# Kernel tuning notes

Hardware: AMD Instinct MI355X
Metric: run time of the kernel (lower is better)

The kernel has to match this reference:

```python
import jax, jax.numpy as jnp
import numpy as np

EMBED_DIM = 1024
NUM_HEADS = 16
HEAD_DIM = EMBED_DIM // NUM_HEADS


def setup_inputs() -> dict:
    key = jax.random.key(0)
    ks = jax.random.split(key, 11)
    B, S, D = 2, 2048, EMBED_DIM
    s = 1.0 / np.sqrt(D)
    inp = {
        "q": jax.random.normal(ks[0], (B, S, D), jnp.float32),
        "k": jax.random.normal(ks[1], (B, S, D), jnp.float32),
        "v": jax.random.normal(ks[2], (B, S, D), jnp.float32),
        # Linear params stored as (in, out) so y = x @ W + b
        "wq": jax.random.uniform(ks[3], (D, D), jnp.float32, -s, s),
        "bq": jax.random.uniform(ks[4], (D,), jnp.float32, -s, s),
        "wk": jax.random.uniform(ks[5], (D, D), jnp.float32, -s, s),
        "bk": jax.random.uniform(ks[6], (D,), jnp.float32, -s, s),
        "wv": jax.random.uniform(ks[7], (D, D), jnp.float32, -s, s),
        "bv": jax.random.uniform(ks[8], (D,), jnp.float32, -s, s),
        "wo": jax.random.uniform(ks[9], (D, D), jnp.float32, -s, s),
        "bo": jax.random.uniform(ks[10], (D,), jnp.float32, -s, s),
    }
    return inp


def reference(q, k, v, wq, bq, wk, bk, wv, bv, wo, bo):
    B, S, D = q.shape
    H, Hd = NUM_HEADS, HEAD_DIM
    temperature = Hd ** 0.5

    def proj(x, w, b):
        # (B, S, D) -> (B, H, S, Hd)
        y = x @ w + b
        return y.reshape(B, S, H, Hd).transpose(0, 2, 1, 3)

    qh = proj(q, wq, bq)
    kh = proj(k, wk, bk)
    vh = proj(v, wv, bv)

    # naive attention with materialized [B, H, S, S] scores (faithful to source)
    scores = jnp.einsum("bhqd,bhkd->bhqk", qh / temperature, kh)
    attn = jax.nn.softmax(scores, axis=-1)
    ctx = jnp.einsum("bhqk,bhkd->bhqd", attn, vh)

    ctx = ctx.transpose(0, 2, 1, 3).reshape(B, S, D)
    out = ctx @ wo + bo
    return out, attn
```

## Files before the change

kernel.cpp:

```cpp
#include <hip/hip_runtime.h>

#define S_   2048
#define D_   1024

typedef __attribute__((ext_vector_type(8))) __bf16 bf16x8;
typedef __attribute__((ext_vector_type(4))) __bf16 bf16x4;
typedef __attribute__((ext_vector_type(4))) float f32x4;
typedef __attribute__((ext_vector_type(4))) float float4v;
typedef __attribute__((ext_vector_type(2))) unsigned int u32x2;
typedef __attribute__((ext_vector_type(4))) unsigned int u32x4;

#define XQ_OFF   0
#define XK_OFF   4194304
#define XV_OFF   8388608
#define WQT_OFF  12582912
#define WKT_OFF  13631488
#define WVT_OFF  14680064
#define WOT_OFF  15728640
#define QH_OFF   16777216
#define KH_OFF   20971520
#define VHT_OFF  25165824
#define CTX_OFF  29360128
#define WS_BYTES 67108864ULL

#if __has_builtin(__builtin_amdgcn_exp2f)
#define EXP2(x) __builtin_amdgcn_exp2f(x)
#else
#define EXP2(x) __expf((x) * 0.69314718056f)
#endif
#define QSCALE 0.1803368801f

__device__ __forceinline__ unsigned short f2b(float f) {
  unsigned u = __builtin_bit_cast(unsigned, f);
  u += 0x7fffu + ((u >> 16) & 1u);
  return (unsigned short)(u >> 16);
}
__device__ __forceinline__ float b2f(unsigned s) {
  return __builtin_bit_cast(float, s << 16);
}

__global__ __launch_bounds__(256) void cvt_all(const float* __restrict__ q,
    const float* __restrict__ k, const float* __restrict__ v,
    const float* __restrict__ wq, const float* __restrict__ wk,
    const float* __restrict__ wv, const float* __restrict__ wo,
    short* __restrict__ ws) {
  __shared__ float tile[32][33];
  int b = blockIdx.x, tid = threadIdx.x;
  if (b < 12288) {
    int y = b >> 12, x = b & 4095;
    const float* src = (y == 0) ? q : (y == 1) ? k : v;
    short* dst = ws + (size_t)y * 4194304;
    size_t t = (size_t)x * 256 + tid;
    float4v f = *(const float4v*)(src + t * 4);
    u32x2 p;
    p[0] = (unsigned)f2b(f[0]) | ((unsigned)f2b(f[1]) << 16);
    p[1] = (unsigned)f2b(f[2]) | ((unsigned)f2b(f[3]) << 16);
    *(u32x2*)(dst + t * 4) = p;
    return;
  }
  int b2 = b - 12288;
  int z = b2 >> 10, rem = b2 & 1023;
  int by = rem >> 5, bx = rem & 31;
  const float* W = (z == 0) ? wq : (z == 1) ? wk : (z == 2) ? wv : wo;
  short* Wt = ws + WQT_OFF + (size_t)z * 1048576;
  int tx = tid & 31, ty = tid >> 5;
#pragma unroll
  for (int i = 0; i < 4; ++i)
    tile[ty + i * 8][tx] =
        W[(size_t)(by * 32 + ty + i * 8) * D_ + bx * 32 + tx];
  __syncthreads();
#pragma unroll
  for (int i = 0; i < 4; ++i)
    Wt[(size_t)(bx * 32 + ty + i * 8) * D_ + by * 32 + tx] =
        (short)f2b(tile[tx][ty + i * 8]);
}

__device__ __forceinline__ void stage_tile(const short* __restrict__ g,
                                           short* l, int w, int lane) {
  int lrow = lane >> 3, lcol = (lane & 7) * 8;
#pragma unroll
  for (int c = 0; c < 4; ++c) {
    int seg = c * 4 + w;
    const short* gp = g + (size_t)(seg * 8 + lrow) * 1024 + lcol;
    short* lp = l + seg * 512 + lane * 8;
    __builtin_amdgcn_global_load_lds(
        (const __attribute__((address_space(1))) void*)gp,
        (__attribute__((address_space(3))) void*)lp, 16, 0, 0);
  }
}

__global__ __launch_bounds__(256) void gemm_bf16(short* __restrict__ ws,
    const float* __restrict__ bq, const float* __restrict__ bk,
    const float* __restrict__ bv, const float* __restrict__ bo,
    float* __restrict__ out, int mode_base) {
  const int tid = threadIdx.x, lane = tid & 63, w = tid >> 6;
  const int wm = w >> 1, wn = w & 1;
  const int ln15 = lane & 15, g = lane >> 4;
  const int bm = blockIdx.y, bn = blockIdx.x;
  const int mode = (mode_base == 3) ? 3 : (int)blockIdx.z;

  const short* A; const short* Bt; const float* bias;
  if (mode == 0)      { A = ws + XQ_OFF;  Bt = ws + WQT_OFF; bias = bq; }
  else if (mode == 1) { A = ws + XK_OFF;  Bt = ws + WKT_OFF; bias = bk; }
  else if (mode == 2) { A = ws + XV_OFF;  Bt = ws + WVT_OFF; bias = bv; }
  else                { A = ws + CTX_OFF; Bt = ws + WOT_OFF; bias = bo; }

  __shared__ short smem[2][2][8192];
  short (*sA)[8192] = smem[0];
  short (*sB)[8192] = smem[1];

  f32x4 acc[4][4] = {};

  const short* Ab = A + (size_t)bm * 128 * 1024;
  const short* Bb = Bt + (size_t)bn * 128 * 1024;

  stage_tile(Ab, sA[0], w, lane);
  stage_tile(Bb, sB[0], w, lane);
  __syncthreads();

  int cur = 0;
#pragma unroll 1
  for (int kt = 0; kt < 16; ++kt) {
    if (kt < 15) {
      stage_tile(Ab + (kt + 1) * 64, sA[cur ^ 1], w, lane);
      stage_tile(Bb + (kt + 1) * 64, sB[cur ^ 1], w, lane);
    }
#pragma unroll
    for (int kk = 0; kk < 2; ++kk) {
      bf16x8 af[4], bfr[4];
#pragma unroll
      for (int m = 0; m < 4; ++m)
        af[m] = *(const bf16x8*)&sA[cur][(wm * 64 + m * 16 + ln15) * 64 + kk * 32 + g * 8];
#pragma unroll
      for (int n = 0; n < 4; ++n)
        bfr[n] = *(const bf16x8*)&sB[cur][(wn * 64 + n * 16 + ln15) * 64 + kk * 32 + g * 8];
#pragma unroll
      for (int m = 0; m < 4; ++m)
#pragma unroll
        for (int n = 0; n < 4; ++n)
          acc[m][n] = __builtin_amdgcn_mfma_f32_16x16x32_bf16(af[m], bfr[n], acc[m][n], 0, 0, 0);
    }
    __syncthreads();
    cur ^= 1;
  }

  float bb[4];
#pragma unroll
  for (int n = 0; n < 4; ++n) bb[n] = bias[bn * 128 + wn * 64 + n * 16 + ln15];

  if (mode == 3) {
#pragma unroll
    for (int m = 0; m < 4; ++m) {
      int row0 = bm * 128 + wm * 64 + m * 16 + g * 4;
#pragma unroll
      for (int n = 0; n < 4; ++n) {
        int col = bn * 128 + wn * 64 + n * 16 + ln15;
#pragma unroll
        for (int r = 0; r < 4; ++r)
          out[(size_t)(row0 + r) * 1024 + col] = acc[m][n][r] + bb[n];
      }
    }
    return;
  }

  float sc = (mode == 0) ? QSCALE : 1.0f;
  short (*tile)[136] = (short(*)[136])smem;
#pragma unroll
  for (int m = 0; m < 4; ++m)
#pragma unroll
    for (int n = 0; n < 4; ++n)
#pragma unroll
      for (int r = 0; r < 4; ++r)
        tile[wm * 64 + m * 16 + g * 4 + r][wn * 64 + n * 16 + ln15] =
            (short)f2b((acc[m][n][r] + bb[n]) * sc);
  __syncthreads();

  if (mode == 2) {
    int dcol = tid >> 1, sh = (tid & 1) * 64;
    int colg = bn * 128 + dcol, h = colg >> 6, hd = colg & 63;
    int b = bm >> 4, sblk = bm & 15;
    short* dst = ws + VHT_OFF +
                 ((size_t)((b * 16 + h) * 16 + sblk)) * 8192 + hd * 128 + sh;
#pragma unroll
    for (int j = 0; j < 8; ++j) {
      u32x4 pk;
#pragma unroll
      for (int q = 0; q < 4; ++q) {
        unsigned lo = (unsigned short)tile[sh + j * 8 + q * 2][dcol];
        unsigned hi = (unsigned short)tile[sh + j * 8 + q * 2 + 1][dcol];
        pk[q] = lo | (hi << 16);
      }
      *(u32x4*)(dst + j * 8) = pk;
    }
  } else {
    int r = tid >> 1, sh = (tid & 1) * 64;
    int colg = bn * 128 + sh, h = colg >> 6;
    int sg = bm * 128 + r, b = sg >> 11, sl = sg & 2047;
    short* dst = ws + ((mode == 0) ? QH_OFF : KH_OFF) +
                 (((size_t)(b * 16 + h)) * 2048 + sl) * 64;
#pragma unroll
    for (int j = 0; j < 8; ++j)
      *(u32x4*)(dst + j * 8) = *(const u32x4*)&tile[r][sh + j * 8];
  }
}

__global__ __launch_bounds__(512) void attn_k(short* __restrict__ ws,
                                              float* __restrict__ attn) {
  const int tid = threadIdx.x, lane = tid & 63, w = tid >> 6;
  const int ln15 = lane & 15, g = lane >> 4, ln7 = lane & 7;
  int bid = blockIdx.x;
  int qt = (bid >> 3) & 15;
  int bh = (bid & 7) + 8 * (bid >> 7);
  const int q0 = qt * 128;

  const short* Q  = ws + QH_OFF  + ((size_t)bh * 2048 + q0) * 64;
  const short* K  = ws + KH_OFF  + (size_t)bh * 2048 * 64;
  const short* Vt = ws + VHT_OFF + (size_t)bh * 131072;

  __shared__ short sStage[6][4096];
  __shared__ short Pbig[128][264];

  const int srow = tid >> 3, sc = tid & 7;
  const int scsw = sc ^ (srow & 7);
  const int sdst = tid * 8;

#define STAGE_K2(kt)                                                          \
  __builtin_amdgcn_global_load_lds(                                           \
      (const __attribute__((address_space(1))) void*)(K + ((kt) * 64 + srow) * 64 + scsw * 8),         \
      (__attribute__((address_space(3))) void*)(&sStage[(kt) % 3][sdst]), 16, 0, 0)
#define STAGE_V2(kt)                                                          \
  __builtin_amdgcn_global_load_lds(                                           \
      (const __attribute__((address_space(1))) void*)(Vt + ((kt) >> 1) * 8192 + srow * 128 + ((kt) & 1) * 64 + scsw * 8), \
      (__attribute__((address_space(3))) void*)(&sStage[3 + (kt) % 3][sdst]), 16, 0, 0)
#define STAGE1(t1, b)                                                         \
  do {                                                                        \
    __builtin_amdgcn_global_load_lds(                                         \
        (const __attribute__((address_space(1))) void*)(K + ((t1) * 128 + srow) * 64 + scsw * 8),      \
        (__attribute__((address_space(3))) void*)(&sStage[(b)][sdst]), 16, 0, 0);                      \
    __builtin_amdgcn_global_load_lds(                                         \
        (const __attribute__((address_space(1))) void*)(K + ((t1) * 128 + 64 + srow) * 64 + scsw * 8), \
        (__attribute__((address_space(3))) void*)(&sStage[3 + (b)][sdst]), 16, 0, 0);                  \
  } while (0)

  bf16x8 qf0 = *(const bf16x8*)&Q[(w * 16 + ln15) * 64 + g * 8];
  bf16x8 qf1 = *(const bf16x8*)&Q[(w * 16 + ln15) * 64 + 32 + g * 8];

  STAGE1(0, 0);
  asm volatile("s_waitcnt vmcnt(0)" ::: "memory");
  __builtin_amdgcn_s_barrier();

  float ps0 = 0.f, ps1 = 0.f;
#pragma unroll 1
  for (int t = 0; t < 16; ++t) {
    int b = t & 1;
    if (t < 15) STAGE1(t + 1, b ^ 1);
#pragma unroll
    for (int m = 0; m < 8; ++m) {
      const short* kbase =
          &sStage[(m >> 2) * 3 + b][((m * 16 + ln15) & 63) * 64];
      bf16x8 ka0 = *(const bf16x8*)&kbase[(g ^ ln7) * 8];
      bf16x8 ka1 = *(const bf16x8*)&kbase[((4 + g) ^ ln7) * 8];
      f32x4 c = {0.f, 0.f, 0.f, 0.f};
      c = __builtin_amdgcn_mfma_f32_16x16x32_bf16(ka0, qf0, c, 0, 0, 0);
      c = __builtin_amdgcn_mfma_f32_16x16x32_bf16(ka1, qf1, c, 0, 0, 0);
      ps0 += EXP2(c[0]) + EXP2(c[1]);
      ps1 += EXP2(c[2]) + EXP2(c[3]);
    }
    asm volatile("s_waitcnt vmcnt(0)" ::: "memory");
    __builtin_amdgcn_s_barrier();
  }
  float ps = ps0 + ps1;
  ps += __shfl_xor(ps, 16, 64);
  ps += __shfl_xor(ps, 32, 64);
  float ri = 1.0f / ps;

  f32x4 cacc[4] = {};

  STAGE_K2(0);
  STAGE_V2(0);
  STAGE_K2(1);
  STAGE_V2(1);
  asm volatile("s_waitcnt vmcnt(2)" ::: "memory");
  __builtin_amdgcn_s_barrier();

#pragma unroll 1
  for (int s = 0; s < 8; ++s) {
#pragma unroll
    for (int j = 0; j < 4; ++j) {
      const int kt = s * 4 + j;
      const int ktm3 = kt % 3;
      if (kt < 30) {
        STAGE_K2(kt + 2);
        STAGE_V2(kt + 2);
      }
#pragma unroll
      for (int m = 0; m < 4; ++m) {
        const short* kbase = &sStage[ktm3][(m * 16 + ln15) * 64];
        bf16x8 ka0 = *(const bf16x8*)&kbase[(g ^ ln7) * 8];
        bf16x8 ka1 = *(const bf16x8*)&kbase[((4 + g) ^ ln7) * 8];
        f32x4 c = {0.f, 0.f, 0.f, 0.f};
        c = __builtin_amdgcn_mfma_f32_16x16x32_bf16(ka0, qf0, c, 0, 0, 0);
        c = __builtin_amdgcn_mfma_f32_16x16x32_bf16(ka1, qf1, c, 0, 0, 0);
        bf16x4 pb;
        pb[0] = (__bf16)(EXP2(c[0]) * ri);
        pb[1] = (__bf16)(EXP2(c[1]) * ri);
        pb[2] = (__bf16)(EXP2(c[2]) * ri);
        pb[3] = (__bf16)(EXP2(c[3]) * ri);
        *(bf16x4*)&Pbig[w * 16 + ln15][j * 64 + m * 16 + g * 4] = pb;
      }
      asm volatile("s_waitcnt lgkmcnt(0)" ::: "memory");
      __builtin_amdgcn_sched_barrier(0);

#pragma unroll
      for (int kk = 0; kk < 2; ++kk) {
        bf16x8 pa =
            *(const bf16x8*)&Pbig[w * 16 + ln15][j * 64 + kk * 32 + g * 8];
#pragma unroll
        for (int n = 0; n < 4; ++n) {
          const short* vbase = &sStage[3 + ktm3][(n * 16 + ln15) * 64];
          bf16x8 vb = *(const bf16x8*)&vbase[((kk * 4 + g) ^ ln7) * 8];
          cacc[n] =
              __builtin_amdgcn_mfma_f32_16x16x32_bf16(pa, vb, cacc[n], 0, 0, 0);
        }
      }

      if (kt >= 30) {
        asm volatile("s_waitcnt vmcnt(0)" ::: "memory");
      } else if (j == 0 && s > 0) {
        asm volatile("s_waitcnt vmcnt(18)" ::: "memory");
      } else {
        asm volatile("s_waitcnt vmcnt(2)" ::: "memory");
      }
      __builtin_amdgcn_s_barrier();
    }

    float* ab = attn + ((size_t)(bh * 2048 + q0 + w * 16)) * 2048 + s * 256 +
                lane * 4;
#pragma unroll
    for (int r = 0; r < 16; ++r) {
      u32x2 pv = *(const u32x2*)&Pbig[w * 16 + r][lane * 4];
      float4v o;
      o[0] = b2f(pv[0] & 0xffffu);
      o[1] = b2f(pv[0] >> 16);
      o[2] = b2f(pv[1] & 0xffffu);
      o[3] = b2f(pv[1] >> 16);
      *(float4v*)(ab + (size_t)r * 2048) = o;
    }
  }

  {
    short* Pw = &Pbig[w * 16][0];
#pragma unroll
    for (int n = 0; n < 4; ++n)
#pragma unroll
      for (int r = 0; r < 4; ++r)
        Pw[(g * 4 + r) * 264 + n * 16 + ln15] = (short)f2b(cacc[n][r]);
    asm volatile("s_waitcnt lgkmcnt(0)" ::: "memory");
    __builtin_amdgcn_sched_barrier(0);
    int b = bh >> 4, h = bh & 15;
    int row = lane >> 3, col = (lane & 7) * 8;
#pragma unroll
    for (int i = 0; i < 2; ++i) {
      int q = q0 + w * 16 + i * 8 + row;
      u32x4 pk = *(const u32x4*)&Pw[(i * 8 + row) * 264 + col];
      *(u32x4*)&ws[CTX_OFF + ((size_t)(b * 2048 + q)) * 1024 + h * 64 + col] = pk;
    }
  }
#undef STAGE_K2
#undef STAGE_V2
#undef STAGE1
}

extern "C" void kernel_launch(void* const* d_in, const int* in_sizes, int n_in,
                              void* d_out, int out_size, void* d_ws, size_t ws_size,
                              hipStream_t stream) {
  const float* q  = (const float*)d_in[0];
  const float* k  = (const float*)d_in[1];
  const float* v  = (const float*)d_in[2];
  const float* wq = (const float*)d_in[3];
  const float* bq = (const float*)d_in[4];
  const float* wk = (const float*)d_in[5];
  const float* bk = (const float*)d_in[6];
  const float* wv = (const float*)d_in[7];
  const float* bv = (const float*)d_in[8];
  const float* wo = (const float*)d_in[9];
  const float* bo = (const float*)d_in[10];
  float* out  = (float*)d_out;
  float* attn = out + 4194304;
  short* ws = (short*)d_ws;
  if (ws_size < WS_BYTES) return;

  cvt_all<<<dim3(16384), 256, 0, stream>>>(q, k, v, wq, wk, wv, wo, ws);
  gemm_bf16<<<dim3(8, 32, 3), 256, 0, stream>>>(ws, bq, bk, bv, bo, out, 0);
  attn_k<<<dim3(512), 512, 0, stream>>>(ws, attn);
  gemm_bf16<<<dim3(8, 32, 1), 256, 0, stream>>>(ws, bq, bk, bv, bo, out, 3);
}
```

Baseline: 294.9 us.

## Store Q/K/V in MFMA fragment order and load fragments directly from global

New measurement: 302.8 us. 2.7% more time.

```diff
diff --git a/kernel.cpp b/kernel.cpp
--- a/kernel.cpp
+++ b/kernel.cpp
@@ -175,99 +175,84 @@
             (short)f2b((acc[m][n][r] + bb[n]) * sc);
   __syncthreads();
 
-  if (mode == 2) {
-    int dcol = tid >> 1, sh = (tid & 1) * 64;
-    int colg = bn * 128 + dcol, h = colg >> 6, hd = colg & 63;
-    int b = bm >> 4, sblk = bm & 15;
-    short* dst = ws + VHT_OFF +
-                 ((size_t)((b * 16 + h) * 16 + sblk)) * 8192 + hd * 128 + sh;
-#pragma unroll
-    for (int j = 0; j < 8; ++j) {
+  const int bq_ = bm >> 4;
+  const int sml = bm & 15;
+  if (mode == 0) {
+    int h_out = tid >> 7, rt = (tid >> 4) & 7, h = (tid >> 3) & 1, sub = tid & 7;
+    int bh = bq_ * 16 + bn * 2 + h_out;
+    size_t base = QH_OFF + (((size_t)bh * 128 + sml * 8 + rt) * 2 + h) * 512;
+#pragma unroll
+    for (int i = 0; i < 8; ++i) {
+      int l = sub * 8 + i;
+      u32x4 v = *(const u32x4*)&tile[rt * 16 + (l & 15)]
+                                    [h_out * 64 + h * 32 + (l >> 4) * 8];
+      *(u32x4*)&ws[base + l * 8] = v;
+    }
+  } else if (mode == 1) {
+    int kt_l = tid >> 7, h_out = (tid >> 6) & 1, f = (tid >> 3) & 7, sub = tid & 7;
+    int bh = bq_ * 16 + bn * 2 + h_out;
+    size_t base = KH_OFF + (((size_t)bh * 32 + sml * 2 + kt_l) * 8 + f) * 512;
+#pragma unroll
+    for (int i = 0; i < 8; ++i) {
+      int l = sub * 8 + i;
+      u32x4 v = *(const u32x4*)&tile[kt_l * 64 + (f >> 1) * 16 + (l & 15)]
+                                    [h_out * 64 + (f & 1) * 32 + (l >> 4) * 8];
+      *(u32x4*)&ws[base + l * 8] = v;
+    }
+  } else {
+    int kt_l = tid >> 7, h_out = (tid >> 6) & 1, fv = (tid >> 3) & 7, sub = tid & 7;
+    int bh = bq_ * 16 + bn * 2 + h_out;
+    size_t base = VHT_OFF + (((size_t)bh * 32 + sml * 2 + kt_l) * 8 + fv) * 512;
+#pragma unroll
+    for (int i = 0; i < 8; ++i) {
+      int l = sub * 8 + i;
+      int hd = h_out * 64 + (fv >> 1) * 16 + (l & 15);
+      int s0 = kt_l * 64 + (fv & 1) * 32 + (l >> 4) * 8;
       u32x4 pk;
 #pragma unroll
-      for (int q = 0; q < 4; ++q) {
-        unsigned lo = (unsigned short)tile[sh + j * 8 + q * 2][dcol];
-        unsigned hi = (unsigned short)tile[sh + j * 8 + q * 2 + 1][dcol];
-        pk[q] = lo | (hi << 16);
+      for (int e2 = 0; e2 < 4; ++e2) {
+        unsigned lo = (unsigned short)tile[s0 + e2 * 2][hd];
+        unsigned hi = (unsigned short)tile[s0 + e2 * 2 + 1][hd];
+        pk[e2] = lo | (hi << 16);
       }
-      *(u32x4*)(dst + j * 8) = pk;
-    }
-  } else {
-    int r = tid >> 1, sh = (tid & 1) * 64;
-    int colg = bn * 128 + sh, h = colg >> 6;
-    int sg = bm * 128 + r, b = sg >> 11, sl = sg & 2047;
-    short* dst = ws + ((mode == 0) ? QH_OFF : KH_OFF) +
-                 (((size_t)(b * 16 + h)) * 2048 + sl) * 64;
-#pragma unroll
-    for (int j = 0; j < 8; ++j)
-      *(u32x4*)(dst + j * 8) = *(const u32x4*)&tile[r][sh + j * 8];
+      *(u32x4*)&ws[base + l * 8] = pk;
+    }
   }
 }
 
 __global__ __launch_bounds__(512) void attn_k(short* __restrict__ ws,
                                               float* __restrict__ attn) {
   const int tid = threadIdx.x, lane = tid & 63, w = tid >> 6;
-  const int ln15 = lane & 15, g = lane >> 4, ln7 = lane & 7;
+  const int ln15 = lane & 15, g = lane >> 4;
   int bid = blockIdx.x;
   int qt = (bid >> 3) & 15;
   int bh = (bid & 7) + 8 * (bid >> 7);
   const int q0 = qt * 128;
 
-  const short* Q  = ws + QH_OFF  + ((size_t)bh * 2048 + q0) * 64;
-  const short* K  = ws + KH_OFF  + (size_t)bh * 2048 * 64;
-  const short* Vt = ws + VHT_OFF + (size_t)bh * 131072;
-
-  __shared__ short sStage[6][4096];
+  const short* qhF = ws + QH_OFF + (((size_t)bh * 128 + qt * 8 + w) * 2) * 512;
+  const short* khF = ws + KH_OFF + (size_t)bh * 131072;
+  const short* vhF = ws + VHT_OFF + (size_t)bh * 131072;
+
   __shared__ short Pbig[128][264];
 
-  const int srow = tid >> 3, sc = tid & 7;
-  const int scsw = sc ^ (srow & 7);
-  const int sdst = tid * 8;
-
-#define STAGE_K2(kt)                                                          \
-  __builtin_amdgcn_global_load_lds(                                           \
-      (const __attribute__((address_space(1))) void*)(K + ((kt) * 64 + srow) * 64 + scsw * 8),         \
-      (__attribute__((address_space(3))) void*)(&sStage[(kt) % 3][sdst]), 16, 0, 0)
-#define STAGE_V2(kt)                                                          \
-  __builtin_amdgcn_global_load_lds(                                           \
-      (const __attribute__((address_space(1))) void*)(Vt + ((kt) >> 1) * 8192 + srow * 128 + ((kt) & 1) * 64 + scsw * 8), \
-      (__attribute__((address_space(3))) void*)(&sStage[3 + (kt) % 3][sdst]), 16, 0, 0)
-#define STAGE1(t1, b)                                                         \
-  do {                                                                        \
-    __builtin_amdgcn_global_load_lds(                                         \
-        (const __attribute__((address_space(1))) void*)(K + ((t1) * 128 + srow) * 64 + scsw * 8),      \
-        (__attribute__((address_space(3))) void*)(&sStage[(b)][sdst]), 16, 0, 0);                      \
-    __builtin_amdgcn_global_load_lds(                                         \
-        (const __attribute__((address_space(1))) void*)(K + ((t1) * 128 + 64 + srow) * 64 + scsw * 8), \
-        (__attribute__((address_space(3))) void*)(&sStage[3 + (b)][sdst]), 16, 0, 0);                  \
-  } while (0)
-
-  bf16x8 qf0 = *(const bf16x8*)&Q[(w * 16 + ln15) * 64 + g * 8];
-  bf16x8 qf1 = *(const bf16x8*)&Q[(w * 16 + ln15) * 64 + 32 + g * 8];
-
-  STAGE1(0, 0);
-  asm volatile("s_waitcnt vmcnt(0)" ::: "memory");
-  __builtin_amdgcn_s_barrier();
+  bf16x8 qf0 = *(const bf16x8*)&qhF[lane * 8];
+  bf16x8 qf1 = *(const bf16x8*)&qhF[512 + lane * 8];
 
   float ps0 = 0.f, ps1 = 0.f;
 #pragma unroll 1
-  for (int t = 0; t < 16; ++t) {
-    int b = t & 1;
-    if (t < 15) STAGE1(t + 1, b ^ 1);
-#pragma unroll
-    for (int m = 0; m < 8; ++m) {
-      const short* kbase =
-          &sStage[(m >> 2) * 3 + b][((m * 16 + ln15) & 63) * 64];
-      bf16x8 ka0 = *(const bf16x8*)&kbase[(g ^ ln7) * 8];
-      bf16x8 ka1 = *(const bf16x8*)&kbase[((4 + g) ^ ln7) * 8];
+  for (int kt = 0; kt < 32; ++kt) {
+    const short* kb = khF + kt * 4096 + lane * 8;
+    bf16x8 ka[8];
+#pragma unroll
+    for (int f = 0; f < 8; ++f) ka[f] = *(const bf16x8*)&kb[f * 512];
+#pragma unroll
+    for (int m = 0; m < 4; ++m) {
       f32x4 c = {0.f, 0.f, 0.f, 0.f};
-      c = __builtin_amdgcn_mfma_f32_16x16x32_bf16(ka0, qf0, c, 0, 0, 0);
-      c = __builtin_amdgcn_mfma_f32_16x16x32_bf16(ka1, qf1, c, 0, 0, 0);
+      c = __builtin_amdgcn_mfma_f32_16x16x32_bf16(ka[m * 2], qf0, c, 0, 0, 0);
+      c = __builtin_amdgcn_mfma_f32_16x16x32_bf16(ka[m * 2 + 1], qf1, c, 0, 0, 0);
       ps0 += EXP2(c[0]) + EXP2(c[1]);
       ps1 += EXP2(c[2]) + EXP2(c[3]);
     }
-    asm volatile("s_waitcnt vmcnt(0)" ::: "memory");
-    __builtin_amdgcn_s_barrier();
   }
   float ps = ps0 + ps1;
   ps += __shfl_xor(ps, 16, 64);
@@ -275,29 +260,16 @@
   float ri = 1.0f / ps;
 
   f32x4 cacc[4] = {};
-
-  STAGE_K2(0);
-  STAGE_V2(0);
-  STAGE_K2(1);
-  STAGE_V2(1);
-  asm volatile("s_waitcnt vmcnt(2)" ::: "memory");
-  __builtin_amdgcn_s_barrier();
-
 #pragma unroll 1
   for (int s = 0; s < 8; ++s) {
 #pragma unroll
     for (int j = 0; j < 4; ++j) {
       const int kt = s * 4 + j;
-      const int ktm3 = kt % 3;
-      if (kt < 30) {
-        STAGE_K2(kt + 2);
-        STAGE_V2(kt + 2);
-      }
+      const short* kb = khF + kt * 4096 + lane * 8;
 #pragma unroll
       for (int m = 0; m < 4; ++m) {
-        const short* kbase = &sStage[ktm3][(m * 16 + ln15) * 64];
-        bf16x8 ka0 = *(const bf16x8*)&kbase[(g ^ ln7) * 8];
-        bf16x8 ka1 = *(const bf16x8*)&kbase[((4 + g) ^ ln7) * 8];
+        bf16x8 ka0 = *(const bf16x8*)&kb[(m * 2) * 512];
+        bf16x8 ka1 = *(const bf16x8*)&kb[(m * 2 + 1) * 512];
         f32x4 c = {0.f, 0.f, 0.f, 0.f};
         c = __builtin_amdgcn_mfma_f32_16x16x32_bf16(ka0, qf0, c, 0, 0, 0);
         c = __builtin_amdgcn_mfma_f32_16x16x32_bf16(ka1, qf1, c, 0, 0, 0);
@@ -308,30 +280,19 @@
         pb[3] = (__bf16)(EXP2(c[3]) * ri);
         *(bf16x4*)&Pbig[w * 16 + ln15][j * 64 + m * 16 + g * 4] = pb;
       }
-      asm volatile("s_waitcnt lgkmcnt(0)" ::: "memory");
-      __builtin_amdgcn_sched_barrier(0);
-
+      const short* vb_ = vhF + kt * 4096 + lane * 8;
+      bf16x8 vb[8];
+#pragma unroll
+      for (int f = 0; f < 8; ++f) vb[f] = *(const bf16x8*)&vb_[f * 512];
 #pragma unroll
       for (int kk = 0; kk < 2; ++kk) {
         bf16x8 pa =
             *(const bf16x8*)&Pbig[w * 16 + ln15][j * 64 + kk * 32 + g * 8];
 #pragma unroll
-        for (int n = 0; n < 4; ++n) {
-          const short* vbase = &sStage[3 + ktm3][(n * 16 + ln15) * 64];
-          bf16x8 vb = *(const bf16x8*)&vbase[((kk * 4 + g) ^ ln7) * 8];
-          cacc[n] =
-              __builtin_amdgcn_mfma_f32_16x16x32_bf16(pa, vb, cacc[n], 0, 0, 0);
-        }
+        for (int n = 0; n < 4; ++n)
+          cacc[n] = __builtin_amdgcn_mfma_f32_16x16x32_bf16(
+              pa, vb[n * 2 + kk], cacc[n], 0, 0, 0);
       }
-
-      if (kt >= 30) {
-        asm volatile("s_waitcnt vmcnt(0)" ::: "memory");
-      } else if (j == 0 && s > 0) {
-        asm volatile("s_waitcnt vmcnt(18)" ::: "memory");
-      } else {
-        asm volatile("s_waitcnt vmcnt(2)" ::: "memory");
-      }
-      __builtin_amdgcn_s_barrier();
     }
 
     float* ab = attn + ((size_t)(bh * 2048 + q0 + w * 16)) * 2048 + s * 256 +
@@ -355,8 +316,6 @@
 #pragma unroll
       for (int r = 0; r < 4; ++r)
         Pw[(g * 4 + r) * 264 + n * 16 + ln15] = (short)f2b(cacc[n][r]);
-    asm volatile("s_waitcnt lgkmcnt(0)" ::: "memory");
-    __builtin_amdgcn_sched_barrier(0);
     int b = bh >> 4, h = bh & 15;
     int row = lane >> 3, col = (lane & 7) * 8;
 #pragma unroll
@@ -366,9 +325,6 @@
       *(u32x4*)&ws[CTX_OFF + ((size_t)(b * 2048 + q)) * 1024 + h * 64 + col] = pk;
     }
   }
-#undef STAGE_K2
-#undef STAGE_V2
-#undef STAGE1
 }
 
 extern "C" void kernel_launch(void* const* d_in, const int* in_sizes, int n_in,
```
